# Optimization experiments

Hardware: AMD Instinct MI355X
Metric: run time of the kernel (lower is better)

## Reference

```python
import jax, jax.numpy as jnp
import numpy as np

H = 128

def setup_inputs() -> dict:
    key = jax.random.key(0)
    ks = jax.random.split(key, 7)
    x = jax.random.normal(ks[0], (4, 65536, H), dtype=jnp.float32)
    # Linear(3H -> H) and Linear(H -> H), torch-style fan-in init scale
    W1 = jax.random.normal(ks[1], (3 * H, H), dtype=jnp.float32) / np.sqrt(3 * H)
    b1 = jax.random.normal(ks[2], (H,), dtype=jnp.float32) * 0.01
    W2 = jax.random.normal(ks[3], (H, H), dtype=jnp.float32) / np.sqrt(H)
    b2 = jax.random.normal(ks[4], (H,), dtype=jnp.float32) * 0.01
    gamma = jnp.ones((H,), dtype=jnp.float32)
    beta = jnp.zeros((H,), dtype=jnp.float32)
    return {"x": x, "W1": W1, "b1": b1, "W2": W2, "b2": b2, "gamma": gamma, "beta": beta}


def _layernorm(h, gamma, beta, eps=1e-5):
    mu = jnp.mean(h, axis=-1, keepdims=True)
    var = jnp.var(h, axis=-1, keepdims=True)
    return (h - mu) * jax.lax.rsqrt(var + eps) * gamma + beta


def reference(x, W1, b1, W2, b2, gamma, beta):
    # circular neighbor gather along node dim
    prev_x = jnp.roll(x, 1, axis=1)
    next_x = jnp.roll(x, -1, axis=1)
    cat = jnp.concatenate([prev_x, x, next_x], axis=-1)  # [B, N, 3H]
    h = jax.nn.relu(jnp.einsum('bnc,ch->bnh', cat, W1) + b1)
    delta = jnp.einsum('bnh,hk->bnk', h, W2) + b2
    return jax.nn.relu(_layernorm(x + delta, gamma, beta))
```

## Files before the change

kernel.cpp:

```cpp
#include <hip/hip_runtime.h>


typedef __bf16 bf16x8 __attribute__((ext_vector_type(8)));
typedef __bf16 bf16x4 __attribute__((ext_vector_type(4)));
typedef float  f32x4  __attribute__((ext_vector_type(4)));

#define H      128
#define NB     65536
#define TILE   64
#define XS     136
#define HSS    136
#define VS     132
#define NTILES 4096

__global__ __launch_bounds__(256, 2)
void cbb_kernel(const float* __restrict__ x, const float* __restrict__ W1,
                const float* __restrict__ b1, const float* __restrict__ W2,
                const float* __restrict__ b2, const float* __restrict__ gamma,
                const float* __restrict__ beta, float* __restrict__ out) {
    __shared__ __align__(16) char raw[(66 * XS + 64 * HSS) * 2];
    __bf16* xs = (__bf16*)raw;
    __bf16* hs = xs + 66 * XS;
    float*  vs = (float*)raw;
    __shared__ float s_mu[64], s_rs[64], s_gamma[128], s_beta[128];

    const int tid  = threadIdx.x;
    const int wid  = tid >> 6;
    const int lane = tid & 63;
    const int l    = lane & 15;
    const int g    = lane >> 4;
    const int col0 = wid * 32;
    const int c0   = col0 + l;
    const int c1   = col0 + 16 + l;

    if (tid < 128) { s_gamma[tid] = gamma[tid]; s_beta[tid] = beta[tid]; }

    const float b1r0 = b1[c0], b1r1 = b1[c1];
    const float b2r0 = b2[c0], b2r1 = b2[c1];

    bf16x8 w1f[12][2];
#pragma unroll
    for (int ks = 0; ks < 12; ++ks) {
#pragma unroll
        for (int ct = 0; ct < 2; ++ct) {
            const int cc = col0 + ct * 16 + l;
            bf16x8 f;
#pragma unroll
            for (int j = 0; j < 8; ++j)
                f[j] = (__bf16)W1[(ks * 32 + g * 8 + j) * H + cc];
            w1f[ks][ct] = f;
        }
    }
    bf16x8 w2f[4][2];
#pragma unroll
    for (int ks = 0; ks < 4; ++ks) {
#pragma unroll
        for (int ct = 0; ct < 2; ++ct) {
            const int cc = col0 + ct * 16 + l;
            bf16x8 f;
#pragma unroll
            for (int j = 0; j < 8; ++j)
                f[j] = (__bf16)W2[(ks * 32 + g * 8 + j) * H + cc];
            w2f[ks][ct] = f;
        }
    }

    for (int t = blockIdx.x; t < NTILES; t += gridDim.x) {
        const int b  = t >> 10;
        const int n0 = (t & 1023) << 6;
        const size_t rowbase = (size_t)b * NB;

        __syncthreads();

        for (int q = tid; q < 66 * 32; q += 256) {
            const int r = q >> 5, c = q & 31;
            const int grow = (n0 - 1 + r + NB) & (NB - 1);
            const float4 f = *(const float4*)(x + ((rowbase + grow) * H + c * 4));
            bf16x4 v4;
            v4[0] = (__bf16)f.x; v4[1] = (__bf16)f.y;
            v4[2] = (__bf16)f.z; v4[3] = (__bf16)f.w;
            *(bf16x4*)(xs + r * XS + c * 4) = v4;
        }
        __syncthreads();

        f32x4 acc[4][2];
#pragma unroll
        for (int rt = 0; rt < 4; ++rt)
#pragma unroll
            for (int ct = 0; ct < 2; ++ct)
                acc[rt][ct] = (f32x4){0.f, 0.f, 0.f, 0.f};

#pragma unroll
        for (int rt = 0; rt < 4; ++rt) {
            const int rb = rt * 16 + l;
#pragma unroll
            for (int ks = 0; ks < 12; ++ks) {
                const int k = ks * 32 + g * 8;
                const bf16x8 a = *(const bf16x8*)(xs + (rb + (k >> 7)) * XS + (k & 127));
                acc[rt][0] = __builtin_amdgcn_mfma_f32_16x16x32_bf16(a, w1f[ks][0], acc[rt][0], 0, 0, 0);
                acc[rt][1] = __builtin_amdgcn_mfma_f32_16x16x32_bf16(a, w1f[ks][1], acc[rt][1], 0, 0, 0);
            }
        }

#pragma unroll
        for (int rt = 0; rt < 4; ++rt) {
#pragma unroll
            for (int i = 0; i < 4; ++i) {
                const int row = rt * 16 + g * 4 + i;
                hs[row * HSS + c0] = (__bf16)fmaxf(acc[rt][0][i] + b1r0, 0.f);
                hs[row * HSS + c1] = (__bf16)fmaxf(acc[rt][1][i] + b1r1, 0.f);
            }
        }
        __syncthreads();

        f32x4 acc2[4][2];
#pragma unroll
        for (int rt = 0; rt < 4; ++rt)
#pragma unroll
            for (int ct = 0; ct < 2; ++ct)
                acc2[rt][ct] = (f32x4){0.f, 0.f, 0.f, 0.f};

#pragma unroll
        for (int rt = 0; rt < 4; ++rt) {
            const int rb = rt * 16 + l;
#pragma unroll
            for (int ks = 0; ks < 4; ++ks) {
                const bf16x8 a = *(const bf16x8*)(hs + rb * HSS + ks * 32 + g * 8);
                acc2[rt][0] = __builtin_amdgcn_mfma_f32_16x16x32_bf16(a, w2f[ks][0], acc2[rt][0], 0, 0, 0);
                acc2[rt][1] = __builtin_amdgcn_mfma_f32_16x16x32_bf16(a, w2f[ks][1], acc2[rt][1], 0, 0, 0);
            }
        }

#pragma unroll
        for (int rt = 0; rt < 4; ++rt) {
#pragma unroll
            for (int i = 0; i < 4; ++i) {
                const int row = rt * 16 + g * 4 + i;
                acc2[rt][0][i] += b2r0 + (float)xs[(row + 1) * XS + c0];
                acc2[rt][1][i] += b2r1 + (float)xs[(row + 1) * XS + c1];
            }
        }
        __syncthreads();

#pragma unroll
        for (int rt = 0; rt < 4; ++rt) {
#pragma unroll
            for (int i = 0; i < 4; ++i) {
                const int row = rt * 16 + g * 4 + i;
                vs[row * VS + c0] = acc2[rt][0][i];
                vs[row * VS + c1] = acc2[rt][1][i];
            }
        }
        __syncthreads();

        {
            const int row = tid >> 2;
            const int cb  = (tid & 3) * 32;
            float s = 0.f, qq = 0.f;
#pragma unroll
            for (int c8 = 0; c8 < 8; ++c8) {
                const f32x4 vv = *(const f32x4*)(vs + row * VS + cb + c8 * 4);
#pragma unroll
                for (int e = 0; e < 4; ++e) { s += vv[e]; qq += vv[e] * vv[e]; }
            }
            s  += __shfl_xor(s, 1, 4);  s  += __shfl_xor(s, 2, 4);
            qq += __shfl_xor(qq, 1, 4); qq += __shfl_xor(qq, 2, 4);
            const float muv = s * (1.f / 128.f);
            const float var = qq * (1.f / 128.f) - muv * muv;
            if ((tid & 3) == 0) { s_mu[row] = muv; s_rs[row] = rsqrtf(var + 1e-5f); }
        }
        __syncthreads();

        {
            const int row = tid >> 2;
            const int cb  = (tid & 3) * 32;
            const float muv = s_mu[row], rv = s_rs[row];
            float* op = out + (rowbase + n0 + row) * H + cb;
#pragma unroll
            for (int c8 = 0; c8 < 8; ++c8) {
                const f32x4 vv = *(const f32x4*)(vs + row * VS + cb + c8 * 4);
                const f32x4 gm = *(const f32x4*)(s_gamma + cb + c8 * 4);
                const f32x4 bt = *(const f32x4*)(s_beta + cb + c8 * 4);
                f32x4 o;
#pragma unroll
                for (int e = 0; e < 4; ++e)
                    o[e] = fmaxf((vv[e] - muv) * rv * gm[e] + bt[e], 0.f);
                *(f32x4*)(op + c8 * 4) = o;
            }
        }
    }
}

extern "C" void kernel_launch(void* const* d_in, const int* in_sizes, int n_in,
                              void* d_out, int out_size, void* d_ws, size_t ws_size,
                              hipStream_t stream) {
    const float* x     = (const float*)d_in[0];
    const float* W1    = (const float*)d_in[1];
    const float* b1    = (const float*)d_in[2];
    const float* W2    = (const float*)d_in[3];
    const float* b2    = (const float*)d_in[4];
    const float* gamma = (const float*)d_in[5];
    const float* beta  = (const float*)d_in[6];
    float* out = (float*)d_out;

    cbb_kernel<<<1024, 256, 0, stream>>>(x, W1, b1, W2, b2, gamma, beta, out);
}
```

Baseline: 302.3 us.

## Register-prefetch next tile, interleave columns, fuse LayerNorm output from accumulators

Loads the next tile's x rows into registers while the current tile's matmuls run, so global-load latency overlaps with MFMA work. Output columns are interleaved (2*l, 2*l+1) so the h and residual staging uses packed 32-bit shared-memory accesses. The final LayerNorm is applied straight from accumulators with 64-bit global stores, which removes one barrier and the reread of vs. Separate LDS buffers replace the aliased layout and the grid is halved to 512 blocks. This raises register pressure by 36 VGPRs for the prefetch and changes the store pattern to narrower, strided writes.

```diff
diff --git a/kernel.cpp b/kernel.cpp
--- a/kernel.cpp
+++ b/kernel.cpp
@@ -4,25 +4,46 @@
 typedef __bf16 bf16x8 __attribute__((ext_vector_type(8)));
 typedef __bf16 bf16x4 __attribute__((ext_vector_type(4)));
 typedef float  f32x4  __attribute__((ext_vector_type(4)));
+typedef float  f32x2  __attribute__((ext_vector_type(2)));
 
 #define H      128
 #define NB     65536
-#define TILE   64
 #define XS     136
 #define HSS    136
 #define VS     132
 #define NTILES 4096
+#define GRID   512
+
+union PK { unsigned u; __bf16 b[2]; };
+
+__device__ __forceinline__ void pf_load(const float* __restrict__ x, int tt, int tid,
+                                        f32x4 pf[9]) {
+    const int n0 = (tt & 1023) << 6;
+    const size_t rowbase = (size_t)(tt >> 10) * NB;
+#pragma unroll
+    for (int i = 0; i < 8; ++i) {
+        const int q = tid + 256 * i;
+        const int r = q >> 5, c = q & 31;
+        const int grow = (n0 - 1 + r + NB) & (NB - 1);
+        pf[i] = *(const f32x4*)(x + ((rowbase + grow) * H + c * 4));
+    }
+    if (tid < 64) {
+        const int q = 2048 + tid;
+        const int r = q >> 5, c = q & 31;
+        const int grow = (n0 - 1 + r + NB) & (NB - 1);
+        pf[8] = *(const f32x4*)(x + ((rowbase + grow) * H + c * 4));
+    }
+}
 
 __global__ __launch_bounds__(256, 2)
 void cbb_kernel(const float* __restrict__ x, const float* __restrict__ W1,
                 const float* __restrict__ b1, const float* __restrict__ W2,
                 const float* __restrict__ b2, const float* __restrict__ gamma,
                 const float* __restrict__ beta, float* __restrict__ out) {
-    __shared__ __align__(16) char raw[(66 * XS + 64 * HSS) * 2];
-    __bf16* xs = (__bf16*)raw;
-    __bf16* hs = xs + 66 * XS;
-    float*  vs = (float*)raw;
-    __shared__ float s_mu[64], s_rs[64], s_gamma[128], s_beta[128];
+    __shared__ __align__(16) __bf16 xs[66 * XS];
+    __shared__ __align__(16) __bf16 hs[64 * HSS];
+    __shared__ __align__(16) float  vs[64 * VS];
+    __shared__ __align__(16) float  s_mu[64], s_rs[64];
 
     const int tid  = threadIdx.x;
     const int wid  = tid >> 6;
@@ -30,20 +51,20 @@
     const int l    = lane & 15;
     const int g    = lane >> 4;
     const int col0 = wid * 32;
-    const int c0   = col0 + l;
-    const int c1   = col0 + 16 + l;
-
-    if (tid < 128) { s_gamma[tid] = gamma[tid]; s_beta[tid] = beta[tid]; }
+    const int c0   = col0 + 2 * l;
+    const int c1   = c0 + 1;
 
     const float b1r0 = b1[c0], b1r1 = b1[c1];
     const float b2r0 = b2[c0], b2r1 = b2[c1];
+    const float gm0  = gamma[c0], gm1 = gamma[c1];
+    const float bt0  = beta[c0],  bt1 = beta[c1];
 
     bf16x8 w1f[12][2];
 #pragma unroll
     for (int ks = 0; ks < 12; ++ks) {
 #pragma unroll
         for (int ct = 0; ct < 2; ++ct) {
-            const int cc = col0 + ct * 16 + l;
+            const int cc = col0 + 2 * l + ct;
             bf16x8 f;
 #pragma unroll
             for (int j = 0; j < 8; ++j)
@@ -56,7 +77,7 @@
     for (int ks = 0; ks < 4; ++ks) {
 #pragma unroll
         for (int ct = 0; ct < 2; ++ct) {
-            const int cc = col0 + ct * 16 + l;
+            const int cc = col0 + 2 * l + ct;
             bf16x8 f;
 #pragma unroll
             for (int j = 0; j < 8; ++j)
@@ -65,23 +86,34 @@
         }
     }
 
-    for (int t = blockIdx.x; t < NTILES; t += gridDim.x) {
-        const int b  = t >> 10;
+    f32x4 pf[9];
+    pf_load(x, blockIdx.x, tid, pf);
+
+    for (int t = blockIdx.x; t < NTILES; t += GRID) {
         const int n0 = (t & 1023) << 6;
-        const size_t rowbase = (size_t)b * NB;
-
-        __syncthreads();
-
-        for (int q = tid; q < 66 * 32; q += 256) {
+        const size_t rowbase = (size_t)(t >> 10) * NB;
+
+#pragma unroll
+        for (int i = 0; i < 8; ++i) {
+            const int q = tid + 256 * i;
             const int r = q >> 5, c = q & 31;
-            const int grow = (n0 - 1 + r + NB) & (NB - 1);
-            const float4 f = *(const float4*)(x + ((rowbase + grow) * H + c * 4));
             bf16x4 v4;
-            v4[0] = (__bf16)f.x; v4[1] = (__bf16)f.y;
-            v4[2] = (__bf16)f.z; v4[3] = (__bf16)f.w;
+            v4[0] = (__bf16)pf[i][0]; v4[1] = (__bf16)pf[i][1];
+            v4[2] = (__bf16)pf[i][2]; v4[3] = (__bf16)pf[i][3];
             *(bf16x4*)(xs + r * XS + c * 4) = v4;
         }
-        __syncthreads();
+        if (tid < 64) {
+            const int q = 2048 + tid;
+            const int r = q >> 5, c = q & 31;
+            bf16x4 v4;
+            v4[0] = (__bf16)pf[8][0]; v4[1] = (__bf16)pf[8][1];
+            v4[2] = (__bf16)pf[8][2]; v4[3] = (__bf16)pf[8][3];
+            *(bf16x4*)(xs + r * XS + c * 4) = v4;
+        }
+        __syncthreads();
+
+        const int tn = (t + GRID < NTILES) ? (t + GRID) : t;
+        pf_load(x, tn, tid, pf);
 
         f32x4 acc[4][2];
 #pragma unroll
@@ -107,8 +139,10 @@
 #pragma unroll
             for (int i = 0; i < 4; ++i) {
                 const int row = rt * 16 + g * 4 + i;
-                hs[row * HSS + c0] = (__bf16)fmaxf(acc[rt][0][i] + b1r0, 0.f);
-                hs[row * HSS + c1] = (__bf16)fmaxf(acc[rt][1][i] + b1r1, 0.f);
+                PK p;
+                p.b[0] = (__bf16)fmaxf(acc[rt][0][i] + b1r0, 0.f);
+                p.b[1] = (__bf16)fmaxf(acc[rt][1][i] + b1r1, 0.f);
+                *(unsigned*)(hs + row * HSS + c0) = p.u;
             }
         }
         __syncthreads();
@@ -136,19 +170,13 @@
 #pragma unroll
             for (int i = 0; i < 4; ++i) {
                 const int row = rt * 16 + g * 4 + i;
-                acc2[rt][0][i] += b2r0 + (float)xs[(row + 1) * XS + c0];
-                acc2[rt][1][i] += b2r1 + (float)xs[(row + 1) * XS + c1];
-            }
-        }
-        __syncthreads();
-
-#pragma unroll
-        for (int rt = 0; rt < 4; ++rt) {
-#pragma unroll
-            for (int i = 0; i < 4; ++i) {
-                const int row = rt * 16 + g * 4 + i;
-                vs[row * VS + c0] = acc2[rt][0][i];
-                vs[row * VS + c1] = acc2[rt][1][i];
+                PK p;
+                p.u = *(const unsigned*)(xs + (row + 1) * XS + c0);
+                const float v0 = acc2[rt][0][i] + b2r0 + (float)p.b[0];
+                const float v1 = acc2[rt][1][i] + b2r1 + (float)p.b[1];
+                acc2[rt][0][i] = v0;
+                acc2[rt][1][i] = v1;
+                *(f32x2*)(vs + row * VS + c0) = (f32x2){v0, v1};
             }
         }
         __syncthreads();
@@ -156,36 +184,33 @@
         {
             const int row = tid >> 2;
             const int cb  = (tid & 3) * 32;
-            float s = 0.f, qq = 0.f;
+            float s = 0.f, q = 0.f;
 #pragma unroll
             for (int c8 = 0; c8 < 8; ++c8) {
                 const f32x4 vv = *(const f32x4*)(vs + row * VS + cb + c8 * 4);
 #pragma unroll
-                for (int e = 0; e < 4; ++e) { s += vv[e]; qq += vv[e] * vv[e]; }
-            }
-            s  += __shfl_xor(s, 1, 4);  s  += __shfl_xor(s, 2, 4);
-            qq += __shfl_xor(qq, 1, 4); qq += __shfl_xor(qq, 2, 4);
-            const float muv = s * (1.f / 128.f);
-            const float var = qq * (1.f / 128.f) - muv * muv;
-            if ((tid & 3) == 0) { s_mu[row] = muv; s_rs[row] = rsqrtf(var + 1e-5f); }
-        }
-        __syncthreads();
-
-        {
-            const int row = tid >> 2;
-            const int cb  = (tid & 3) * 32;
-            const float muv = s_mu[row], rv = s_rs[row];
-            float* op = out + (rowbase + n0 + row) * H + cb;
-#pragma unroll
-            for (int c8 = 0; c8 < 8; ++c8) {
-                const f32x4 vv = *(const f32x4*)(vs + row * VS + cb + c8 * 4);
-                const f32x4 gm = *(const f32x4*)(s_gamma + cb + c8 * 4);
-                const f32x4 bt = *(const f32x4*)(s_beta + cb + c8 * 4);
-                f32x4 o;
-#pragma unroll
-                for (int e = 0; e < 4; ++e)
-                    o[e] = fmaxf((vv[e] - muv) * rv * gm[e] + bt[e], 0.f);
-                *(f32x4*)(op + c8 * 4) = o;
+                for (int e = 0; e < 4; ++e) { s += vv[e]; q += vv[e] * vv[e]; }
+            }
+            s += __shfl_xor(s, 1); s += __shfl_xor(s, 2);
+            q += __shfl_xor(q, 1); q += __shfl_xor(q, 2);
+            if ((tid & 3) == 0) {
+                const float muv = s * (1.f / 128.f);
+                s_mu[row] = muv;
+                s_rs[row] = rsqrtf(q * (1.f / 128.f) - muv * muv + 1e-5f);
+            }
+        }
+        __syncthreads();
+
+#pragma unroll
+        for (int rt = 0; rt < 4; ++rt) {
+            const int r0 = rt * 16 + g * 4;
+            const f32x4 mu4 = *(const f32x4*)(s_mu + r0);
+            const f32x4 rs4 = *(const f32x4*)(s_rs + r0);
+#pragma unroll
+            for (int i = 0; i < 4; ++i) {
+                const float o0 = fmaxf((acc2[rt][0][i] - mu4[i]) * rs4[i] * gm0 + bt0, 0.f);
+                const float o1 = fmaxf((acc2[rt][1][i] - mu4[i]) * rs4[i] * gm1 + bt1, 0.f);
+                *(f32x2*)(out + (rowbase + n0 + r0 + i) * H + c0) = (f32x2){o0, o1};
             }
         }
     }
@@ -203,5 +228,5 @@
     const float* beta  = (const float*)d_in[6];
     float* out = (float*)d_out;
 
-    cbb_kernel<<<1024, 256, 0, stream>>>(x, W1, b1, W2, b2, gamma, beta, out);
+    cbb_kernel<<<GRID, 256, 0, stream>>>(x, W1, b1, W2, b2, gamma, beta, out);
 }
```

New measurement: 331.5 us. 9.6% more time.
